# Kernel optimization log

Hardware: AMD Instinct MI355X
Metric: run time of the kernel (lower is better)

## Reference

```python
import jax, jax.numpy as jnp
import numpy as np
from jax import lax

S, B, F, H = 2048, 512, 1, 128  # seq_len, minibatch, feature_count, mlp hidden


def setup_inputs() -> dict:
    key = jax.random.key(0)
    ks = jax.random.split(key, 7)
    x = jax.random.normal(ks[0], (S, B, F), dtype=jnp.float32)
    # derivative network: 2 -> H -> H -> 2 tanh MLP (ignores t, as in repo)
    W1 = jax.random.normal(ks[1], (2, H), dtype=jnp.float32) / np.sqrt(2.0)
    b1 = jnp.zeros((H,), dtype=jnp.float32)
    W2 = jax.random.normal(ks[2], (H, H), dtype=jnp.float32) / np.sqrt(H)
    b2 = jnp.zeros((H,), dtype=jnp.float32)
    W3 = jax.random.normal(ks[3], (H, 2), dtype=jnp.float32) / np.sqrt(H)
    b3 = jnp.zeros((2,), dtype=jnp.float32)
    return {"x": x, "W1": W1, "b1": b1, "W2": W2, "b2": b2, "W3": W3, "b3": b3}


def reference(x, W1, b1, W2, b2, W3, b3):
    # x: (S, B, 1). Per step n: v = [x_n, state] in R^2 per sequence,
    # one forward-Euler step with dt = (n) - (n-1) = 1.0:
    #   y1 = v + dt * f(v)
    # output_n = y1[..., 1]; state <- output_n. Strict sequential recurrence.
    def mlp(v):  # v: (B, 2)
        h = jnp.tanh(v @ W1 + b1)
        h = jnp.tanh(h @ W2 + b2)
        return h @ W3 + b3  # (B, 2)

    dt = jnp.float32(1.0)

    def step(state, x_n):  # state: (B,1), x_n: (B,1)
        v = jnp.concatenate([x_n, state], axis=1)  # (B, 2)
        y1 = v + dt * mlp(v)
        out = y1[:, 1:2]  # channel 1 of the 2-dim ODE state
        return out, out

    init = jnp.zeros((x.shape[1], 1), dtype=x.dtype)
    _, ys = lax.scan(step, init, x)  # (S, B, 1)
    return ys
```

## Files before the change

kernel.cpp:

```cpp
#include <hip/hip_runtime.h>

#define SEQ 2048
#define BATCH 512
#define HDIM 128

typedef __bf16 bf16x8 __attribute__((ext_vector_type(8)));
typedef float  f32x4  __attribute__((ext_vector_type(4)));
typedef unsigned int uint32;

__device__ __forceinline__ float tanh_e2(float y) {
    float e;
    asm("v_exp_f32 %0, %1" : "=v"(e) : "v"(y));
    return fmaf(-2.0f, __builtin_amdgcn_rcpf(e + 1.0f), 1.0f);
}

template<int CTRL>
__device__ __forceinline__ float dpp_add(float x) {
    return x + __int_as_float(__builtin_amdgcn_update_dpp(
        0, __float_as_int(x), CTRL, 0xf, 0xf, true));
}

__global__ __launch_bounds__(256, 2)
void odenet_scan_kernel(const float* __restrict__ x,
                        const float* __restrict__ W1,
                        const float* __restrict__ b1,
                        const float* __restrict__ W2,
                        const float* __restrict__ b2,
                        const float* __restrict__ W3,
                        const float* __restrict__ b3,
                        float* __restrict__ out)
{
    const int t  = threadIdx.x;
    const int l  = t & 63;
    const int wv = t >> 6;
    const int b  = blockIdx.x;

    constexpr float CS = 2.8853900817779268f;

    __shared__ float xbuf[SEQ];
    __shared__ unsigned short hbuf[4][2][144];
    __shared__ __align__(16) float ybuf[2][4];

    #pragma unroll
    for (int i = 0; i < 8; ++i)
        xbuf[i * 256 + t] = x[(i * 256 + t) * BATCH + b];

    bf16x8 Bhi[2][4], Blo[2][4];
    #pragma unroll
    for (int nt = 0; nt < 2; ++nt) {
        #pragma unroll
        for (int kt = 0; kt < 4; ++kt) {
            union { unsigned short u[8]; bf16x8 v; } fh, fl;
            #pragma unroll
            for (int j = 0; j < 8; ++j) {
                const int k = 32 * kt + 8 * (l >> 4) + j;
                const int c = 32 * wv + 16 * nt + (l & 15);
                const float v = W2[k * HDIM + c] * CS;
                const uint32 u = __float_as_uint(v);
                fh.u[j] = (unsigned short)(u >> 16);
                const float hif = __uint_as_float(u & 0xffff0000u);
                fl.u[j] = (unsigned short)(__float_as_uint(v - hif) >> 16);
            }
            Bhi[nt][kt] = fh.v;
            Blo[nt][kt] = fl.v;
        }
    }

    const float2 w1x_ = *reinterpret_cast<const float2*>(&W1[2 * l]);
    const float2 w1s_ = *reinterpret_cast<const float2*>(&W1[HDIM + 2 * l]);
    const float2 b1v_ = *reinterpret_cast<const float2*>(&b1[2 * l]);
    const float2 w1x = make_float2(w1x_.x * CS, w1x_.y * CS);
    const float2 w1s = make_float2(w1s_.x * CS, w1s_.y * CS);
    const float2 b1v = make_float2(b1v_.x * CS, b1v_.y * CS);

    const int cz = 32 * wv + (l & 15);
    const float b2a = b2[cz] * CS,  b2b = b2[cz + 16] * CS;
    const float w3a = W3[2 * cz + 1], w3b = W3[2 * (cz + 16) + 1];
    const float b31 = b3[1];

    uint32* pWh = reinterpret_cast<uint32*>(&hbuf[wv][0][2 * l]);
    uint32* pWl = reinterpret_cast<uint32*>(&hbuf[wv][1][2 * l]);
    const int rowe = ((l & 15) == 0) ? 0 : 1;
    const unsigned short* pA = &hbuf[wv][rowe][8 * (l >> 4)];

    __syncthreads();

    float s = 0.0f, s_hold = 0.0f;
    float xn = xbuf[0];
    float2 pre1 = make_float2(fmaf(w1x.x, xn, b1v.x), fmaf(w1x.y, xn, b1v.y));

    for (int n = 0; n < SEQ; ++n) {
        const int par = n & 1;

        const float h0 = tanh_e2(fmaf(w1s.x, s, pre1.x));
        const float h1 = tanh_e2(fmaf(w1s.y, s, pre1.y));
        const uint32 u0 = __float_as_uint(h0), u1 = __float_as_uint(h1);
        const uint32 hi01 = __builtin_amdgcn_perm(u1, u0, 0x07060302u);
        const float r0 = h0 - __uint_as_float(u0 & 0xffff0000u);
        const float r1 = h1 - __uint_as_float(u1 & 0xffff0000u);
        const uint32 lo01 = __builtin_amdgcn_perm(
            __float_as_uint(r1), __float_as_uint(r0), 0x07060302u);
        *pWh = hi01;
        *pWl = lo01;
        __builtin_amdgcn_wave_barrier();

        const float xnext = xbuf[(n + 1) & (SEQ - 1)];
        pre1 = make_float2(fmaf(w1x.x, xnext, b1v.x), fmaf(w1x.y, xnext, b1v.y));

        f32x4 Ch0 = {b2a, b2a, b2a, b2a};
        f32x4 Ch1 = {b2b, b2b, b2b, b2b};
        f32x4 Cl0 = {0.0f, 0.0f, 0.0f, 0.0f};
        f32x4 Cl1 = {0.0f, 0.0f, 0.0f, 0.0f};
        #pragma unroll
        for (int kt = 0; kt < 4; ++kt) {
            const bf16x8 a = __builtin_bit_cast(bf16x8,
                *reinterpret_cast<const uint4*>(pA + 32 * kt));
            Ch0 = __builtin_amdgcn_mfma_f32_16x16x32_bf16(a, Bhi[0][kt], Ch0, 0, 0, 0);
            Ch1 = __builtin_amdgcn_mfma_f32_16x16x32_bf16(a, Bhi[1][kt], Ch1, 0, 0, 0);
            Cl0 = __builtin_amdgcn_mfma_f32_16x16x32_bf16(a, Blo[0][kt], Cl0, 0, 0, 0);
            Cl1 = __builtin_amdgcn_mfma_f32_16x16x32_bf16(a, Blo[1][kt], Cl1, 0, 0, 0);
        }
        __builtin_amdgcn_wave_barrier();

        const float p0 = (Ch0[0] + Ch0[1]) + Cl0[0];
        const float p1 = (Ch1[0] + Ch1[1]) + Cl1[0];
        float z = fmaf(tanh_e2(p1), w3b, tanh_e2(p0) * w3a);

        z = dpp_add<0xB1>(z);
        z = dpp_add<0x4E>(z);
        z = dpp_add<0x141>(z);
        z = dpp_add<0x140>(z);

        if (l == 0) ybuf[par][wv] = z;
        __syncthreads();

        const float4 yv = *reinterpret_cast<const float4*>(&ybuf[par][0]);
        s += ((yv.x + yv.y) + (yv.z + yv.w)) + b31;

        if (wv == 0) {
            if (l == (n & 63)) s_hold = s;
            if ((n & 63) == 63) out[(n - 63 + l) * BATCH + b] = s_hold;
        }
        xn = xnext;
    }
}

extern "C" void kernel_launch(void* const* d_in, const int* in_sizes, int n_in,
                              void* d_out, int out_size, void* d_ws, size_t ws_size,
                              hipStream_t stream) {
    const float* x  = (const float*)d_in[0];
    const float* W1 = (const float*)d_in[1];
    const float* b1 = (const float*)d_in[2];
    const float* W2 = (const float*)d_in[3];
    const float* b2 = (const float*)d_in[4];
    const float* W3 = (const float*)d_in[5];
    const float* b3 = (const float*)d_in[6];
    float* out = (float*)d_out;

    dim3 grid(BATCH);
    dim3 block(256);
    odenet_scan_kernel<<<grid, block, 0, stream>>>(x, W1, b1, W2, b2, W3, b3, out);
}
```

Before: 936.4 us.

## Process two sequences per block with 8 waves each owning 16 hidden columns

```diff
diff --git a/kernel.cpp b/kernel.cpp
--- a/kernel.cpp
+++ b/kernel.cpp
@@ -20,7 +20,7 @@
         0, __float_as_int(x), CTRL, 0xf, 0xf, true));
 }
 
-__global__ __launch_bounds__(256, 2)
+__global__ __launch_bounds__(512, 1)
 void odenet_scan_kernel(const float* __restrict__ x,
                         const float* __restrict__ W1,
                         const float* __restrict__ b1,
@@ -33,37 +33,34 @@
     const int t  = threadIdx.x;
     const int l  = t & 63;
     const int wv = t >> 6;
-    const int b  = blockIdx.x;
+    const int b0 = 2 * blockIdx.x;
 
     constexpr float CS = 2.8853900817779268f;
 
-    __shared__ float xbuf[SEQ];
-    __shared__ unsigned short hbuf[4][2][144];
-    __shared__ __align__(16) float ybuf[2][4];
+    __shared__ float2 xbuf[SEQ];
+    __shared__ unsigned short hbuf[8][4 * 144];
+    __shared__ __align__(16) float2 ybuf[2][8];
 
     #pragma unroll
-    for (int i = 0; i < 8; ++i)
-        xbuf[i * 256 + t] = x[(i * 256 + t) * BATCH + b];
+    for (int i = 0; i < 4; ++i)
+        xbuf[i * 512 + t] = *reinterpret_cast<const float2*>(&x[(i * 512 + t) * BATCH + b0]);
 
-    bf16x8 Bhi[2][4], Blo[2][4];
+    bf16x8 Bhi[4], Blo[4];
+    const int bc = 16 * wv + (l & 15);
     #pragma unroll
-    for (int nt = 0; nt < 2; ++nt) {
+    for (int kt = 0; kt < 4; ++kt) {
+        union { unsigned short u[8]; bf16x8 v; } fh, fl;
         #pragma unroll
-        for (int kt = 0; kt < 4; ++kt) {
-            union { unsigned short u[8]; bf16x8 v; } fh, fl;
-            #pragma unroll
-            for (int j = 0; j < 8; ++j) {
-                const int k = 32 * kt + 8 * (l >> 4) + j;
-                const int c = 32 * wv + 16 * nt + (l & 15);
-                const float v = W2[k * HDIM + c] * CS;
-                const uint32 u = __float_as_uint(v);
-                fh.u[j] = (unsigned short)(u >> 16);
-                const float hif = __uint_as_float(u & 0xffff0000u);
-                fl.u[j] = (unsigned short)(__float_as_uint(v - hif) >> 16);
-            }
-            Bhi[nt][kt] = fh.v;
-            Blo[nt][kt] = fl.v;
+        for (int j = 0; j < 8; ++j) {
+            const int k = 32 * kt + 8 * (l >> 4) + j;
+            const float v = W2[k * HDIM + bc] * CS;
+            const uint32 u = __float_as_uint(v);
+            fh.u[j] = (unsigned short)(u >> 16);
+            const float hif = __uint_as_float(u & 0xffff0000u);
+            fl.u[j] = (unsigned short)(__float_as_uint(v - hif) >> 16);
         }
+        Bhi[kt] = fh.v;
+        Blo[kt] = fl.v;
     }
 
     const float2 w1x_ = *reinterpret_cast<const float2*>(&W1[2 * l]);
@@ -73,75 +70,86 @@
     const float2 w1s = make_float2(w1s_.x * CS, w1s_.y * CS);
     const float2 b1v = make_float2(b1v_.x * CS, b1v_.y * CS);
 
-    const int cz = 32 * wv + (l & 15);
-    const float b2a = b2[cz] * CS,  b2b = b2[cz + 16] * CS;
-    const float w3a = W3[2 * cz + 1], w3b = W3[2 * (cz + 16) + 1];
+    const float b2v = b2[bc] * CS;
+    const float w3v = W3[2 * bc + 1];
     const float b31 = b3[1];
 
-    uint32* pWh = reinterpret_cast<uint32*>(&hbuf[wv][0][2 * l]);
-    uint32* pWl = reinterpret_cast<uint32*>(&hbuf[wv][1][2 * l]);
-    const int rowe = ((l & 15) == 0) ? 0 : 1;
-    const unsigned short* pA = &hbuf[wv][rowe][8 * (l >> 4)];
+    uint32* pW0 = reinterpret_cast<uint32*>(&hbuf[wv][0 * 144 + 2 * l]);
+    uint32* pW1 = reinterpret_cast<uint32*>(&hbuf[wv][1 * 144 + 2 * l]);
+    uint32* pW2 = reinterpret_cast<uint32*>(&hbuf[wv][2 * 144 + 2 * l]);
+    uint32* pW3 = reinterpret_cast<uint32*>(&hbuf[wv][3 * 144 + 2 * l]);
+    const unsigned short* pA = &hbuf[wv][(l & 3) * 144 + 8 * (l >> 4)];
 
     __syncthreads();
 
-    float s = 0.0f, s_hold = 0.0f;
-    float xn = xbuf[0];
-    float2 pre1 = make_float2(fmaf(w1x.x, xn, b1v.x), fmaf(w1x.y, xn, b1v.y));
+    float sA = 0.0f, sB = 0.0f, s_hold = 0.0f;
+    const float2 x0 = xbuf[0];
+    float2 p1A = make_float2(fmaf(w1x.x, x0.x, b1v.x), fmaf(w1x.y, x0.x, b1v.y));
+    float2 p1B = make_float2(fmaf(w1x.x, x0.y, b1v.x), fmaf(w1x.y, x0.y, b1v.y));
 
     for (int n = 0; n < SEQ; ++n) {
         const int par = n & 1;
 
-        const float h0 = tanh_e2(fmaf(w1s.x, s, pre1.x));
-        const float h1 = tanh_e2(fmaf(w1s.y, s, pre1.y));
-        const uint32 u0 = __float_as_uint(h0), u1 = __float_as_uint(h1);
-        const uint32 hi01 = __builtin_amdgcn_perm(u1, u0, 0x07060302u);
-        const float r0 = h0 - __uint_as_float(u0 & 0xffff0000u);
-        const float r1 = h1 - __uint_as_float(u1 & 0xffff0000u);
-        const uint32 lo01 = __builtin_amdgcn_perm(
-            __float_as_uint(r1), __float_as_uint(r0), 0x07060302u);
-        *pWh = hi01;
-        *pWl = lo01;
+        const float hA0 = tanh_e2(fmaf(w1s.x, sA, p1A.x));
+        const float hA1 = tanh_e2(fmaf(w1s.y, sA, p1A.y));
+        const float hB0 = tanh_e2(fmaf(w1s.x, sB, p1B.x));
+        const float hB1 = tanh_e2(fmaf(w1s.y, sB, p1B.y));
+        const uint32 uA0 = __float_as_uint(hA0), uA1 = __float_as_uint(hA1);
+        const uint32 uB0 = __float_as_uint(hB0), uB1 = __float_as_uint(hB1);
+        const uint32 hiA = __builtin_amdgcn_perm(uA1, uA0, 0x07060302u);
+        const uint32 hiB = __builtin_amdgcn_perm(uB1, uB0, 0x07060302u);
+        const float rA0 = hA0 - __uint_as_float(uA0 & 0xffff0000u);
+        const float rA1 = hA1 - __uint_as_float(uA1 & 0xffff0000u);
+        const float rB0 = hB0 - __uint_as_float(uB0 & 0xffff0000u);
+        const float rB1 = hB1 - __uint_as_float(uB1 & 0xffff0000u);
+        const uint32 loA = __builtin_amdgcn_perm(
+            __float_as_uint(rA1), __float_as_uint(rA0), 0x07060302u);
+        const uint32 loB = __builtin_amdgcn_perm(
+            __float_as_uint(rB1), __float_as_uint(rB0), 0x07060302u);
+        *pW0 = hiA; *pW1 = loA; *pW2 = hiB; *pW3 = loB;
         __builtin_amdgcn_wave_barrier();
 
-        const float xnext = xbuf[(n + 1) & (SEQ - 1)];
-        pre1 = make_float2(fmaf(w1x.x, xnext, b1v.x), fmaf(w1x.y, xnext, b1v.y));
+        const float2 xn2 = xbuf[(n + 1) & (SEQ - 1)];
+        p1A = make_float2(fmaf(w1x.x, xn2.x, b1v.x), fmaf(w1x.y, xn2.x, b1v.y));
+        p1B = make_float2(fmaf(w1x.x, xn2.y, b1v.x), fmaf(w1x.y, xn2.y, b1v.y));
 
-        f32x4 Ch0 = {b2a, b2a, b2a, b2a};
-        f32x4 Ch1 = {b2b, b2b, b2b, b2b};
-        f32x4 Cl0 = {0.0f, 0.0f, 0.0f, 0.0f};
-        f32x4 Cl1 = {0.0f, 0.0f, 0.0f, 0.0f};
+        f32x4 Ch = {0.0f, 0.0f, 0.0f, 0.0f};
+        f32x4 Cl = {0.0f, 0.0f, 0.0f, 0.0f};
         #pragma unroll
         for (int kt = 0; kt < 4; ++kt) {
             const bf16x8 a = __builtin_bit_cast(bf16x8,
                 *reinterpret_cast<const uint4*>(pA + 32 * kt));
-            Ch0 = __builtin_amdgcn_mfma_f32_16x16x32_bf16(a, Bhi[0][kt], Ch0, 0, 0, 0);
-            Ch1 = __builtin_amdgcn_mfma_f32_16x16x32_bf16(a, Bhi[1][kt], Ch1, 0, 0, 0);
-            Cl0 = __builtin_amdgcn_mfma_f32_16x16x32_bf16(a, Blo[0][kt], Cl0, 0, 0, 0);
-            Cl1 = __builtin_amdgcn_mfma_f32_16x16x32_bf16(a, Blo[1][kt], Cl1, 0, 0, 0);
+            Ch = __builtin_amdgcn_mfma_f32_16x16x32_bf16(a, Bhi[kt], Ch, 0, 0, 0);
+            Cl = __builtin_amdgcn_mfma_f32_16x16x32_bf16(a, Blo[kt], Cl, 0, 0, 0);
         }
         __builtin_amdgcn_wave_barrier();
 
-        const float p0 = (Ch0[0] + Ch0[1]) + Cl0[0];
-        const float p1 = (Ch1[0] + Ch1[1]) + Cl1[0];
-        float z = fmaf(tanh_e2(p1), w3b, tanh_e2(p0) * w3a);
+        const float pAv = (Ch[0] + Ch[1]) + (Cl[0] + b2v);
+        const float pBv = (Ch[2] + Ch[3]) + (Cl[2] + b2v);
+        float zA = tanh_e2(pAv) * w3v;
+        float zB = tanh_e2(pBv) * w3v;
 
-        z = dpp_add<0xB1>(z);
-        z = dpp_add<0x4E>(z);
-        z = dpp_add<0x141>(z);
-        z = dpp_add<0x140>(z);
+        zA = dpp_add<0xB1>(zA);   zB = dpp_add<0xB1>(zB);
+        zA = dpp_add<0x4E>(zA);   zB = dpp_add<0x4E>(zB);
+        zA = dpp_add<0x141>(zA);  zB = dpp_add<0x141>(zB);
+        zA = dpp_add<0x140>(zA);  zB = dpp_add<0x140>(zB);
 
-        if (l == 0) ybuf[par][wv] = z;
+        if (l == 0) ybuf[par][wv] = make_float2(zA, zB);
         __syncthreads();
 
-        const float4 yv = *reinterpret_cast<const float4*>(&ybuf[par][0]);
-        s += ((yv.x + yv.y) + (yv.z + yv.w)) + b31;
+        const float4* yq = reinterpret_cast<const float4*>(&ybuf[par][0]);
+        const float4 q0 = yq[0], q1 = yq[1], q2 = yq[2], q3 = yq[3];
+        const float dyA = ((q0.x + q0.z) + (q1.x + q1.z))
+                        + ((q2.x + q2.z) + (q3.x + q3.z)) + b31;
+        const float dyB = ((q0.y + q0.w) + (q1.y + q1.w))
+                        + ((q2.y + q2.w) + (q3.y + q3.w)) + b31;
+        sA += dyA;
+        sB += dyB;
 
-        if (wv == 0) {
-            if (l == (n & 63)) s_hold = s;
-            if ((n & 63) == 63) out[(n - 63 + l) * BATCH + b] = s_hold;
+        if (wv < 2) {
+            if (l == (n & 63)) s_hold = wv ? sB : sA;
+            if ((n & 63) == 63) out[(n - 63 + l) * BATCH + b0 + wv] = s_hold;
         }
-        xn = xnext;
     }
 }
 
@@ -157,7 +165,7 @@
     const float* b3 = (const float*)d_in[6];
     float* out = (float*)d_out;
 
-    dim3 grid(BATCH);
-    dim3 block(256);
+    dim3 grid(BATCH / 2);
+    dim3 block(512);
     odenet_scan_kernel<<<grid, block, 0, stream>>>(x, W1, b1, W2, b2, W3, b3, out);
 }
```

Measured after the change: 1.165 ms. 1.24x slower.

## Split hidden-layer MFMA across eight waves with shared hidden-state buffer

Applied to the files above, without the earlier changes.

```diff
diff --git a/kernel.cpp b/kernel.cpp
--- a/kernel.cpp
+++ b/kernel.cpp
@@ -20,7 +20,7 @@
         0, __float_as_int(x), CTRL, 0xf, 0xf, true));
 }
 
-__global__ __launch_bounds__(256, 2)
+__global__ __launch_bounds__(512, 4)
 void odenet_scan_kernel(const float* __restrict__ x,
                         const float* __restrict__ W1,
                         const float* __restrict__ b1,
@@ -38,110 +38,99 @@
     constexpr float CS = 2.8853900817779268f;
 
     __shared__ float xbuf[SEQ];
-    __shared__ unsigned short hbuf[4][2][144];
-    __shared__ __align__(16) float ybuf[2][4];
+    __shared__ unsigned short hbuf[2][144];
+    __shared__ __align__(16) float ybuf[8];
 
     #pragma unroll
-    for (int i = 0; i < 8; ++i)
-        xbuf[i * 256 + t] = x[(i * 256 + t) * BATCH + b];
+    for (int i = 0; i < 4; ++i)
+        xbuf[i * 512 + t] = x[(i * 512 + t) * BATCH + b];
 
-    bf16x8 Bhi[2][4], Blo[2][4];
+    bf16x8 Bhi[4], Blo[4];
+    const int bc = 16 * wv + (l & 15);
     #pragma unroll
-    for (int nt = 0; nt < 2; ++nt) {
+    for (int kt = 0; kt < 4; ++kt) {
+        union { unsigned short u[8]; bf16x8 v; } fh, fl;
         #pragma unroll
-        for (int kt = 0; kt < 4; ++kt) {
-            union { unsigned short u[8]; bf16x8 v; } fh, fl;
-            #pragma unroll
-            for (int j = 0; j < 8; ++j) {
-                const int k = 32 * kt + 8 * (l >> 4) + j;
-                const int c = 32 * wv + 16 * nt + (l & 15);
-                const float v = W2[k * HDIM + c] * CS;
-                const uint32 u = __float_as_uint(v);
-                fh.u[j] = (unsigned short)(u >> 16);
-                const float hif = __uint_as_float(u & 0xffff0000u);
-                fl.u[j] = (unsigned short)(__float_as_uint(v - hif) >> 16);
-            }
-            Bhi[nt][kt] = fh.v;
-            Blo[nt][kt] = fl.v;
+        for (int j = 0; j < 8; ++j) {
+            const int k = 32 * kt + 8 * (l >> 4) + j;
+            const float v = W2[k * HDIM + bc] * CS;
+            const uint32 u = __float_as_uint(v);
+            fh.u[j] = (unsigned short)(u >> 16);
+            const float hif = __uint_as_float(u & 0xffff0000u);
+            fl.u[j] = (unsigned short)(__float_as_uint(v - hif) >> 16);
         }
+        Bhi[kt] = fh.v;
+        Blo[kt] = fl.v;
     }
 
-    const float2 w1x_ = *reinterpret_cast<const float2*>(&W1[2 * l]);
-    const float2 w1s_ = *reinterpret_cast<const float2*>(&W1[HDIM + 2 * l]);
-    const float2 b1v_ = *reinterpret_cast<const float2*>(&b1[2 * l]);
-    const float2 w1x = make_float2(w1x_.x * CS, w1x_.y * CS);
-    const float2 w1s = make_float2(w1s_.x * CS, w1s_.y * CS);
-    const float2 b1v = make_float2(b1v_.x * CS, b1v_.y * CS);
-
-    const int cz = 32 * wv + (l & 15);
-    const float b2a = b2[cz] * CS,  b2b = b2[cz + 16] * CS;
-    const float w3a = W3[2 * cz + 1], w3b = W3[2 * (cz + 16) + 1];
+    const float b2v = b2[bc] * CS;
+    const float w3v = W3[2 * bc + 1];
     const float b31 = b3[1];
 
-    uint32* pWh = reinterpret_cast<uint32*>(&hbuf[wv][0][2 * l]);
-    uint32* pWl = reinterpret_cast<uint32*>(&hbuf[wv][1][2 * l]);
+    float w1xv = 0.0f, w1sv = 0.0f, b1vv = 0.0f;
+    if (t < 128) {
+        w1xv = W1[t] * CS;
+        w1sv = W1[HDIM + t] * CS;
+        b1vv = b1[t] * CS;
+    }
+
     const int rowe = ((l & 15) == 0) ? 0 : 1;
-    const unsigned short* pA = &hbuf[wv][rowe][8 * (l >> 4)];
+    const unsigned short* pA = &hbuf[rowe][8 * (l >> 4)];
 
     __syncthreads();
 
     float s = 0.0f, s_hold = 0.0f;
-    float xn = xbuf[0];
-    float2 pre1 = make_float2(fmaf(w1x.x, xn, b1v.x), fmaf(w1x.y, xn, b1v.y));
+
+    if (t < 128) {
+        const float h = tanh_e2(fmaf(w1xv, xbuf[0], b1vv));
+        const uint32 u = __float_as_uint(h);
+        hbuf[0][t] = (unsigned short)(u >> 16);
+        const float hf = __uint_as_float(u & 0xffff0000u);
+        hbuf[1][t] = (unsigned short)(__float_as_uint(h - hf) >> 16);
+    }
+    __syncthreads();
 
     for (int n = 0; n < SEQ; ++n) {
-        const int par = n & 1;
+        float pre1 = 0.0f;
+        if (t < 128)
+            pre1 = fmaf(w1xv, xbuf[(n + 1) & (SEQ - 1)], b1vv);
 
-        const float h0 = tanh_e2(fmaf(w1s.x, s, pre1.x));
-        const float h1 = tanh_e2(fmaf(w1s.y, s, pre1.y));
-        const uint32 u0 = __float_as_uint(h0), u1 = __float_as_uint(h1);
-        const uint32 hi01 = __builtin_amdgcn_perm(u1, u0, 0x07060302u);
-        const float r0 = h0 - __uint_as_float(u0 & 0xffff0000u);
-        const float r1 = h1 - __uint_as_float(u1 & 0xffff0000u);
-        const uint32 lo01 = __builtin_amdgcn_perm(
-            __float_as_uint(r1), __float_as_uint(r0), 0x07060302u);
-        *pWh = hi01;
-        *pWl = lo01;
-        __builtin_amdgcn_wave_barrier();
-
-        const float xnext = xbuf[(n + 1) & (SEQ - 1)];
-        pre1 = make_float2(fmaf(w1x.x, xnext, b1v.x), fmaf(w1x.y, xnext, b1v.y));
-
-        f32x4 Ch0 = {b2a, b2a, b2a, b2a};
-        f32x4 Ch1 = {b2b, b2b, b2b, b2b};
-        f32x4 Cl0 = {0.0f, 0.0f, 0.0f, 0.0f};
-        f32x4 Cl1 = {0.0f, 0.0f, 0.0f, 0.0f};
+        f32x4 Ch = {0.0f, 0.0f, 0.0f, 0.0f};
+        f32x4 Cl = {0.0f, 0.0f, 0.0f, 0.0f};
         #pragma unroll
         for (int kt = 0; kt < 4; ++kt) {
             const bf16x8 a = __builtin_bit_cast(bf16x8,
                 *reinterpret_cast<const uint4*>(pA + 32 * kt));
-            Ch0 = __builtin_amdgcn_mfma_f32_16x16x32_bf16(a, Bhi[0][kt], Ch0, 0, 0, 0);
-            Ch1 = __builtin_amdgcn_mfma_f32_16x16x32_bf16(a, Bhi[1][kt], Ch1, 0, 0, 0);
-            Cl0 = __builtin_amdgcn_mfma_f32_16x16x32_bf16(a, Blo[0][kt], Cl0, 0, 0, 0);
-            Cl1 = __builtin_amdgcn_mfma_f32_16x16x32_bf16(a, Blo[1][kt], Cl1, 0, 0, 0);
+            Ch = __builtin_amdgcn_mfma_f32_16x16x32_bf16(a, Bhi[kt], Ch, 0, 0, 0);
+            Cl = __builtin_amdgcn_mfma_f32_16x16x32_bf16(a, Blo[kt], Cl, 0, 0, 0);
         }
-        __builtin_amdgcn_wave_barrier();
-
-        const float p0 = (Ch0[0] + Ch0[1]) + Cl0[0];
-        const float p1 = (Ch1[0] + Ch1[1]) + Cl1[0];
-        float z = fmaf(tanh_e2(p1), w3b, tanh_e2(p0) * w3a);
-
+        const float p = (Ch[0] + Ch[1]) + (Cl[0] + b2v);
+        float z = tanh_e2(p) * w3v;
         z = dpp_add<0xB1>(z);
         z = dpp_add<0x4E>(z);
         z = dpp_add<0x141>(z);
         z = dpp_add<0x140>(z);
-
-        if (l == 0) ybuf[par][wv] = z;
+        if (l == 0) ybuf[wv] = z;
         __syncthreads();
 
-        const float4 yv = *reinterpret_cast<const float4*>(&ybuf[par][0]);
-        s += ((yv.x + yv.y) + (yv.z + yv.w)) + b31;
+        if (t < 128) {
+            const float4 y0 = *reinterpret_cast<const float4*>(&ybuf[0]);
+            const float4 y1 = *reinterpret_cast<const float4*>(&ybuf[4]);
+            s += ((y0.x + y0.y) + (y0.z + y0.w))
+               + ((y1.x + y1.y) + (y1.z + y1.w)) + b31;
 
-        if (wv == 0) {
-            if (l == (n & 63)) s_hold = s;
-            if ((n & 63) == 63) out[(n - 63 + l) * BATCH + b] = s_hold;
+            if (t < 64) {
+                if (l == (n & 63)) s_hold = s;
+                if ((n & 63) == 63) out[(n - 63 + l) * BATCH + b] = s_hold;
+            }
+
+            const float h = tanh_e2(fmaf(w1sv, s, pre1));
+            const uint32 u = __float_as_uint(h);
+            hbuf[0][t] = (unsigned short)(u >> 16);
+            const float hf = __uint_as_float(u & 0xffff0000u);
+            hbuf[1][t] = (unsigned short)(__float_as_uint(h - hf) >> 16);
         }
-        xn = xnext;
+        __syncthreads();
     }
 }
 
@@ -158,6 +147,6 @@
     float* out = (float*)d_out;
 
     dim3 grid(BATCH);
-    dim3 block(256);
+    dim3 block(512);
     odenet_scan_kernel<<<grid, block, 0, stream>>>(x, W1, b1, W2, b2, W3, b3, out);
 }
```

Result: slower. 988.0 us (+5.5%).
